# Kernel optimization log

Hardware: AMD Instinct MI355X
Metric: run time of the kernel (lower is better)

The kernel has to match this reference:

```python
import jax, jax.numpy as jnp
import numpy as np

N_NODES = 40000
N_EDGES = 640000
HIDDEN = 128
N_LAYERS = 4
N_CLASSES = 40
SCALING = HIDDEN ** -0.5  # num_heads = 1 -> head_dim = HIDDEN


def setup_inputs() -> dict:
    key = jax.random.key(0)
    ks = jax.random.split(key, 8)
    w_scale = HIDDEN ** -0.5
    h = jax.random.normal(ks[0], (N_NODES, HIDDEN), dtype=jnp.float32)
    src = jax.random.randint(ks[1], (N_EDGES,), 0, N_NODES, dtype=jnp.int32)
    dst = jnp.sort(jax.random.randint(ks[2], (N_EDGES,), 0, N_NODES, dtype=jnp.int32))
    Wq = jax.random.normal(ks[3], (N_LAYERS, HIDDEN, HIDDEN), dtype=jnp.float32) * w_scale
    Wk = jax.random.normal(ks[4], (N_LAYERS, HIDDEN, HIDDEN), dtype=jnp.float32) * w_scale
    Wv = jax.random.normal(ks[5], (N_LAYERS, HIDDEN, HIDDEN), dtype=jnp.float32) * w_scale
    bq = jnp.zeros((N_LAYERS, HIDDEN), dtype=jnp.float32)
    bk = jnp.zeros((N_LAYERS, HIDDEN), dtype=jnp.float32)
    bv = jnp.zeros((N_LAYERS, HIDDEN), dtype=jnp.float32)
    Wout = jax.random.normal(ks[6], (HIDDEN, N_CLASSES), dtype=jnp.float32) * w_scale
    bout = jnp.zeros((N_CLASSES,), dtype=jnp.float32)
    return {"h": h, "src": src, "dst": dst, "Wq": Wq, "bq": bq, "Wk": Wk,
            "bk": bk, "Wv": Wv, "bv": bv, "Wout": Wout, "bout": bout}


def _edge_softmax_spmm(q, k, v, src, dst):
    """Sparse MHA over graph edges (num_heads=1).
    score_e = <q[dst_e], k[src_e]>, softmax over incoming edges per dst,
    out[i] = sum_{e: dst_e = i} attn_e * v[src_e].
    """
    # SDDMM: [E]
    score = jnp.einsum('ed,ed->e', q[dst], k[src])
    # edge softmax over destination segments (stable)
    m = jax.ops.segment_max(score, dst, num_segments=N_NODES)  # [N]
    e = jnp.exp(score - m[dst])                                # [E]
    s = jax.ops.segment_sum(e, dst, num_segments=N_NODES)      # [N]
    attn = e / jnp.maximum(s[dst], 1e-20)                      # [E]
    # SpMM: [N, d]
    return jax.ops.segment_sum(attn[:, None] * v[src], dst, num_segments=N_NODES)


def reference(h, src, dst, Wq, bq, Wk, bk, Wv, bv, Wout, bout):
    for l in range(N_LAYERS):
        q = (h @ Wq[l] + bq[l]) * SCALING
        k = h @ Wk[l] + bk[l]
        v = h @ Wv[l] + bv[l]
        h = _edge_softmax_spmm(q, k, v, src, dst)
    logits = h @ Wout + bout
    return jax.nn.log_softmax(logits, axis=-1)
```

## Files before the change

kernel.cpp:

```cpp
#include <hip/hip_runtime.h>
#include <math.h>

#define N_NODES 40000
#define N_EDGES 640000
#define HIDDEN 128
#define N_LAYERS 4
#define N_CLASSES 40
#define SCALING 0.08838834764831845f

typedef __attribute__((ext_vector_type(8))) short short8;
typedef __attribute__((ext_vector_type(4))) float floatx4;

static __device__ __forceinline__ float b2f(unsigned short u) {
  return __uint_as_float(((unsigned)u) << 16);
}
static __device__ __forceinline__ unsigned short f2b(float f) {
  unsigned u = __float_as_uint(f);
  u += 0x7fff + ((u >> 16) & 1);
  return (unsigned short)(u >> 16);
}

__global__ __launch_bounds__(256) void setup_all(
    const float* __restrict__ h_in, const int* __restrict__ dst,
    const float* __restrict__ Wq, const float* __restrict__ Wk,
    const float* __restrict__ Wv, const float* __restrict__ Wout,
    unsigned short* __restrict__ hb0, int* __restrict__ row_start,
    unsigned short* __restrict__ Wqb, unsigned short* __restrict__ Wkb,
    unsigned short* __restrict__ Wvb, unsigned short* __restrict__ W2buf,
    unsigned short* __restrict__ wout_t)
{
  int idx = blockIdx.x * 256 + threadIdx.x;
  if (idx < 640000) {
    const float4* p = (const float4*)h_in + (size_t)idx * 2;
    float4 a = p[0], b = p[1];
    union { unsigned short us[8]; uint4 v; } o;
    o.us[0] = f2b(a.x); o.us[1] = f2b(a.y); o.us[2] = f2b(a.z); o.us[3] = f2b(a.w);
    o.us[4] = f2b(b.x); o.us[5] = f2b(b.y); o.us[6] = f2b(b.z); o.us[7] = f2b(b.w);
    ((uint4*)hb0)[idx] = o.v;
    return;
  }
  int j = idx - 640000;
  if (j < 65536) { Wqb[j] = f2b(Wq[j]); return; }
  if (j < 131072) { int i = j - 65536; Wkb[i] = f2b(Wk[i]); return; }
  if (j < 196608) { int i = j - 131072; Wvb[i] = f2b(Wv[i]); return; }
  if (j < 245760) {
    int i = j - 196608;
    int l = i >> 14, rem = i & 16383;
    int d = rem >> 7, kk = rem & 127;
    W2buf[(size_t)l * 32768 + (size_t)d * 128 + kk] =
        f2b(Wv[(size_t)l * 16384 + (size_t)kk * 128 + d]);
    return;
  }
  if (j < 251904) {
    int i = j - 245760;
    int c = i >> 7, d = i & 127;
    wout_t[i] = (c < N_CLASSES) ? f2b(Wout[(size_t)d * N_CLASSES + c]) : 0;
    return;
  }
  int c = j - 251904;
  if (c <= N_NODES) {
    int lo = 0, hi = N_EDGES;
    while (lo < hi) {
      int mid = (lo + hi) >> 1;
      if (dst[mid] < c) lo = mid + 1; else hi = mid;
    }
    row_start[c] = lo;
  }
}

__device__ __forceinline__ void mm_body(
    const unsigned short* __restrict__ Aop, const unsigned short* __restrict__ Bop,
    unsigned short* __restrict__ outp, int n_b, float scale)
{
  const int wid = threadIdx.x >> 6, lane = threadIdx.x & 63;
  const int r = lane & 15, kg = lane >> 4;
  const int row_base = wid * 32;

  int br0 = row_base + r;      if (br0 > n_b - 1) br0 = n_b - 1;
  int br1 = row_base + 16 + r; if (br1 > n_b - 1) br1 = n_b - 1;

  short8 bf_[2][4];
  #pragma unroll
  for (int kc = 0; kc < 4; ++kc) {
    bf_[0][kc] = *(const short8*)(Bop + (size_t)br0 * 128 + kc * 32 + kg * 8);
    bf_[1][kc] = *(const short8*)(Bop + (size_t)br1 * 128 + kc * 32 + kg * 8);
  }

  floatx4 acc[8][2];
  #pragma unroll
  for (int df = 0; df < 8; ++df) {
    acc[df][0] = (floatx4){0.f, 0.f, 0.f, 0.f};
    acc[df][1] = (floatx4){0.f, 0.f, 0.f, 0.f};
  }

  const unsigned short* ap = Aop + (size_t)r * 128 + kg * 8;
  #pragma unroll
  for (int df = 0; df < 8; ++df) {
    #pragma unroll
    for (int kc = 0; kc < 4; ++kc) {
      short8 af = *(const short8*)(ap + df * 2048 + kc * 32);
      acc[df][0] = __builtin_amdgcn_mfma_f32_16x16x32_bf16(af, bf_[0][kc], acc[df][0], 0, 0, 0);
      acc[df][1] = __builtin_amdgcn_mfma_f32_16x16x32_bf16(af, bf_[1][kc], acc[df][1], 0, 0, 0);
    }
  }

  #pragma unroll
  for (int df = 0; df < 8; ++df) {
    #pragma unroll
    for (int f = 0; f < 2; ++f) {
      int b = row_base + f * 16 + r;
      if (b < n_b) {
        union { unsigned short us[4]; uint2 u2; } o;
        o.us[0] = f2b(acc[df][f][0] * scale);
        o.us[1] = f2b(acc[df][f][1] * scale);
        o.us[2] = f2b(acc[df][f][2] * scale);
        o.us[3] = f2b(acc[df][f][3] * scale);
        *(uint2*)(outp + (size_t)b * 128 + df * 16 + kg * 4) = o.u2;
      }
    }
  }
}

__global__ __launch_bounds__(256) void mm_stage1(
    const unsigned short* __restrict__ Wqb, const unsigned short* __restrict__ Wkb,
    unsigned short* __restrict__ mts)
{
  int l = blockIdx.x;
  mm_body(Wqb + (size_t)l * 16384, Wkb + (size_t)l * 16384,
          mts + (size_t)l * 16384, 128, SCALING);
}

__global__ __launch_bounds__(256) void stage2_bias(
    const unsigned short* __restrict__ mts, const unsigned short* __restrict__ Wvb,
    const unsigned short* __restrict__ wout_t,
    unsigned short* __restrict__ W2buf, unsigned short* __restrict__ wout2,
    const float* __restrict__ bq, const float* __restrict__ Wk,
    const float* __restrict__ bv, const float* __restrict__ Wout,
    const float* __restrict__ bout,
    float* __restrict__ bqk0, float* __restrict__ bias2, float* __restrict__ bout2)
{
  int job = blockIdx.x;
  if (job < 3) {
    int l = job + 1;
    mm_body(Wvb + (size_t)(l - 1) * 16384, mts + (size_t)l * 16384,
            W2buf + (size_t)(l - 1) * 32768 + 16384, 128, 1.0f);
    return;
  }
  if (job == 3) {
    mm_body(Wvb + (size_t)3 * 16384, wout_t, wout2, 48, 1.0f);
    return;
  }
  int idx = (job - 4) * 256 + threadIdx.x;
  if (idx < 128) {
    int tp = idx;
    const float* wkrow = Wk + (size_t)tp * 128;
    float s = 0.f;
    #pragma unroll 4
    for (int j = 0; j < 128; ++j) s += bq[j] * wkrow[j];
    bqk0[tp] = s * SCALING;
  } else if (idx < 512) {
    int i = idx - 128;
    int l = (i >> 7) + 1, tp = i & 127;
    const unsigned short* mrow = mts + (size_t)l * 16384 + (size_t)tp * 128;
    const float* bvp = bv + (size_t)(l - 1) * 128;
    float s = 0.f;
    #pragma unroll 4
    for (int t = 0; t < 128; ++t) s += bvp[t] * b2f(mrow[t]);
    const float* bqp = bq + (size_t)l * 128;
    const float* wkrow = Wk + (size_t)l * 16384 + (size_t)tp * 128;
    float s2 = 0.f;
    #pragma unroll 4
    for (int j = 0; j < 128; ++j) s2 += bqp[j] * wkrow[j];
    bias2[(size_t)(l - 1) * 256 + 128 + tp] = s + s2 * SCALING;
  } else if (idx < 896) {
    int i = idx - 512;
    int l = (i >> 7) + 1, d = i & 127;
    bias2[(size_t)(l - 1) * 256 + d] = bv[(size_t)(l - 1) * 128 + d];
  } else if (idx < 944) {
    int c = idx - 896;
    float s = 0.f;
    #pragma unroll 4
    for (int d = 0; d < 128; ++d) s += bv[3 * 128 + d] * Wout[(size_t)d * N_CLASSES + c];
    bout2[c] = s + bout[c];
  }
}

template<int NCOLS>
__global__ __launch_bounds__(256) void gemm_qn(
    const unsigned short* __restrict__ A,
    const unsigned short* __restrict__ Wt,
    const float* __restrict__ bias,
    unsigned short* __restrict__ C)
{
  constexpr int HALF = NCOLS / 2;
  constexpr int NDF = HALF / 16;
  constexpr int ROWB = NCOLS * 2;
  __shared__ __align__(16) unsigned char cs[32 * ROWB];

  const int tid = threadIdx.x;
  const int wid = tid >> 6, lane = tid & 63;
  const int r = lane & 15, kg = lane >> 4;
  const int colhalf = wid & 1, rowsub = wid >> 1;
  const int colbase = colhalf * HALF;
  const int ro = rowsub * 16 + r;
  const int row = blockIdx.x * 32 + ro;

  short8 hf[4];
  #pragma unroll
  for (int kc = 0; kc < 4; ++kc)
    hf[kc] = *(const short8*)(A + (size_t)row * 128 + kc * 32 + kg * 8);

  floatx4 acc[NDF];
  #pragma unroll
  for (int df = 0; df < NDF; ++df) acc[df] = (floatx4){0.f, 0.f, 0.f, 0.f};

  const unsigned short* wp = Wt + (size_t)(colbase + r) * 128 + kg * 8;
  #pragma unroll
  for (int df = 0; df < NDF; ++df) {
    #pragma unroll
    for (int kc = 0; kc < 4; ++kc) {
      short8 wf = *(const short8*)(wp + df * 2048 + kc * 32);
      acc[df] = __builtin_amdgcn_mfma_f32_16x16x32_bf16(wf, hf[kc], acc[df], 0, 0, 0);
    }
  }

  #pragma unroll
  for (int df = 0; df < NDF; ++df) {
    float4 b4 = *(const float4*)&bias[colbase + df * 16 + kg * 4];
    union { unsigned short us[4]; uint2 u2; } o;
    o.us[0] = f2b(acc[df][0] + b4.x);
    o.us[1] = f2b(acc[df][1] + b4.y);
    o.us[2] = f2b(acc[df][2] + b4.z);
    o.us[3] = f2b(acc[df][3] + b4.w);
    int colb = (colbase + df * 16 + kg * 4) * 2;
    *(uint2*)(cs + ro * ROWB + (colb ^ ((ro & 7) << 4))) = o.u2;
  }
  __syncthreads();

  unsigned char* dstb = (unsigned char*)(C + (size_t)blockIdx.x * 32 * NCOLS);
  constexpr int NV = 32 * ROWB / 16;
  #pragma unroll
  for (int i = 0; i < NV / 256; ++i) {
    int byte = (i * 256 + tid) * 16;
    int ro2 = byte / ROWB;
    int colb2 = byte & (ROWB - 1);
    *(uint4*)(dstb + byte) =
        *(const uint4*)(cs + ro2 * ROWB + (colb2 ^ ((ro2 & 7) << 4)));
  }
}

template<int QSH, int HSH>
__global__ __launch_bounds__(128) void edge_fused(
    const unsigned short* __restrict__ qm, const unsigned short* __restrict__ h,
    const int* __restrict__ src, const int* __restrict__ row_start,
    unsigned short* __restrict__ g)
{
  const int lane = threadIdx.x & 63;
  const int node = blockIdx.x * 2 + (threadIdx.x >> 6);
  const int sg = lane >> 4, sl = lane & 15;

  short8 qf = *(const short8*)(qm + ((size_t)node << QSH) + sl * 8);
  float qd[8];
  #pragma unroll
  for (int j = 0; j < 8; ++j) qd[j] = b2f((unsigned short)qf[j]);

  const int r0 = row_start[node], r1 = row_start[node + 1];

  float acc[8] = {0.f, 0.f, 0.f, 0.f, 0.f, 0.f, 0.f, 0.f};
  float ws = 0.f;

#define LOADG(VLD, HF, C)                                               \
  {                                                                     \
    int e_ = (C) + sg;                                                  \
    VLD = e_ < r1;                                                      \
    int s_ = VLD ? src[e_] : 0;                                         \
    HF = *(const short8*)(h + ((size_t)s_ << HSH) + sl * 8);            \
  }

#define COMPG(VLD, HF)                                                  \
  {                                                                     \
    float hd_[8];                                                       \
    _Pragma("unroll")                                                   \
    for (int j = 0; j < 8; ++j) hd_[j] = b2f((unsigned short)HF[j]);    \
    float d0_ = 0.f, d1_ = 0.f;                                         \
    _Pragma("unroll")                                                   \
    for (int j = 0; j < 4; ++j) d0_ += qd[j] * hd_[j];                  \
    _Pragma("unroll")                                                   \
    for (int j = 4; j < 8; ++j) d1_ += qd[j] * hd_[j];                  \
    float d_ = d0_ + d1_;                                               \
    d_ += __shfl_xor(d_, 1, 64);                                        \
    d_ += __shfl_xor(d_, 2, 64);                                        \
    d_ += __shfl_xor(d_, 4, 64);                                        \
    d_ += __shfl_xor(d_, 8, 64);                                        \
    float w_ = VLD ? __expf(d_) : 0.f;                                  \
    ws += w_;                                                           \
    _Pragma("unroll")                                                   \
    for (int j = 0; j < 8; ++j) acc[j] += w_ * hd_[j];                  \
  }

  bool vA, vB;
  short8 hA, hB;
  LOADG(vA, hA, r0);
  LOADG(vB, hB, r0 + 4);

  for (int c = r0; c < r1; c += 8) {
    bool vC, vD;
    short8 hC, hD;
    LOADG(vC, hC, c + 8);
    LOADG(vD, hD, c + 12);
    COMPG(vA, hA);
    COMPG(vB, hB);
    vA = vC; hA = hC;
    vB = vD; hB = hD;
  }

#undef LOADG
#undef COMPG

  #pragma unroll
  for (int off = 16; off <= 32; off <<= 1) {
    ws += __shfl_xor(ws, off, 64);
    #pragma unroll
    for (int j = 0; j < 8; ++j) acc[j] += __shfl_xor(acc[j], off, 64);
  }

  if (sg == 0) {
    float inv = (ws > 1e-20f) ? 1.0f / ws : 0.0f;
    union { unsigned short us[8]; uint4 u4; } o;
    #pragma unroll
    for (int j = 0; j < 8; ++j) o.us[j] = f2b(acc[j] * inv);
    *(uint4*)(g + (size_t)node * 128 + sl * 8) = o.u4;
  }
}

__global__ __launch_bounds__(256) void out_head_mfma(
    const unsigned short* __restrict__ h, const unsigned short* __restrict__ wout_t,
    const float* __restrict__ bout, float* __restrict__ out)
{
  __shared__ __align__(16) float os[64 * N_CLASSES];

  const int wid = threadIdx.x >> 6, lane = threadIdx.x & 63;
  const int r = lane & 15, kg = lane >> 4;
  const int row_base = blockIdx.x * 64 + wid * 16;
  const int ar = row_base + r;

  floatx4 acc[3];
  #pragma unroll
  for (int n = 0; n < 3; ++n) acc[n] = (floatx4){0.f, 0.f, 0.f, 0.f};

  const unsigned short* ap = h + (size_t)ar * 128 + kg * 8;
  const unsigned short* bp = wout_t + (size_t)r * 128 + kg * 8;

  #pragma unroll
  for (int kc = 0; kc < 128; kc += 32) {
    short8 a0 = *(const short8*)(ap + kc);
    #pragma unroll
    for (int n = 0; n < 3; ++n) {
      short8 b = *(const short8*)(bp + n * 2048 + kc);
      acc[n] = __builtin_amdgcn_mfma_f32_16x16x32_bf16(a0, b, acc[n], 0, 0, 0);
    }
  }

  float bn0 = bout[r];
  float bn1 = bout[16 + r];
  float bn2 = (r < 8) ? bout[32 + r] : 0.f;

  #pragma unroll
  for (int g = 0; g < 4; ++g) {
    int rl = wid * 16 + kg * 4 + g;
    float l0 = acc[0][g] + bn0;
    float l1 = acc[1][g] + bn1;
    float l2 = acc[2][g] + bn2;
    float m = fmaxf(l0, l1);
    if (r < 8) m = fmaxf(m, l2);
    #pragma unroll
    for (int off = 8; off >= 1; off >>= 1) m = fmaxf(m, __shfl_xor(m, off, 64));
    float s = __expf(l0 - m) + __expf(l1 - m) + ((r < 8) ? __expf(l2 - m) : 0.f);
    #pragma unroll
    for (int off = 8; off >= 1; off >>= 1) s += __shfl_xor(s, off, 64);
    float lse = m + logf(s);
    os[rl * N_CLASSES + r]      = l0 - lse;
    os[rl * N_CLASSES + 16 + r] = l1 - lse;
    if (r < 8) os[rl * N_CLASSES + 32 + r] = l2 - lse;
  }
  __syncthreads();

  float* dstb = out + (size_t)blockIdx.x * 64 * N_CLASSES;
  #pragma unroll
  for (int i = 0; i < 3; ++i) {
    int idx = i * 256 + threadIdx.x;
    if (idx < 640)
      *(uint4*)(dstb + idx * 4) = *(const uint4*)(os + idx * 4);
  }
}

extern "C" void kernel_launch(void* const* d_in, const int* in_sizes, int n_in,
                              void* d_out, int out_size, void* d_ws, size_t ws_size,
                              hipStream_t stream) {
  const float* h_in = (const float*)d_in[0];
  const int*   src  = (const int*)d_in[1];
  const int*   dst  = (const int*)d_in[2];
  const float* Wq   = (const float*)d_in[3];
  const float* bq   = (const float*)d_in[4];
  const float* Wk   = (const float*)d_in[5];
  const float* bk   = (const float*)d_in[6];
  const float* Wv   = (const float*)d_in[7];
  const float* bv   = (const float*)d_in[8];
  const float* Wout = (const float*)d_in[9];
  const float* bout = (const float*)d_in[10];
  float* out = (float*)d_out;
  (void)bk;

  char* ws = (char*)d_ws;
  size_t off = 0;
  auto alloc = [&](size_t bytes) -> void* {
    void* p = ws + off;
    off += (bytes + 255) & ~(size_t)255;
    return p;
  };
  int*            row_start = (int*)           alloc((size_t)(N_NODES + 1) * sizeof(int));
  unsigned short* hb0       = (unsigned short*)alloc((size_t)N_NODES * 128 * 2);
  unsigned short* qm0       = (unsigned short*)alloc((size_t)N_NODES * 128 * 2);
  unsigned short* g0        = (unsigned short*)alloc((size_t)N_NODES * 128 * 2);
  unsigned short* g1        = (unsigned short*)alloc((size_t)N_NODES * 128 * 2);
  unsigned short* hq        = (unsigned short*)alloc((size_t)N_NODES * 256 * 2);
  unsigned short* mts       = (unsigned short*)alloc((size_t)4 * 16384 * 2);
  unsigned short* W2buf     = (unsigned short*)alloc((size_t)3 * 32768 * 2);
  unsigned short* wout2     = (unsigned short*)alloc((size_t)48 * 128 * 2);
  unsigned short* Wqb       = (unsigned short*)alloc((size_t)4 * 16384 * 2);
  unsigned short* Wkb       = (unsigned short*)alloc((size_t)4 * 16384 * 2);
  unsigned short* Wvb       = (unsigned short*)alloc((size_t)4 * 16384 * 2);
  unsigned short* wout_t    = (unsigned short*)alloc((size_t)48 * 128 * 2);
  float*          bqk0      = (float*)         alloc(128 * sizeof(float));
  float*          bias2     = (float*)         alloc(3 * 256 * sizeof(float));
  float*          bout2     = (float*)         alloc(48 * sizeof(float));

  setup_all<<<3641, 256, 0, stream>>>(h_in, dst, Wq, Wk, Wv, Wout,
                                      hb0, row_start, Wqb, Wkb, Wvb, W2buf, wout_t);
  mm_stage1<<<4, 256, 0, stream>>>(Wqb, Wkb, mts);
  stage2_bias<<<8, 256, 0, stream>>>(mts, Wvb, wout_t, W2buf, wout2,
                                     bq, Wk, bv, Wout, bout, bqk0, bias2, bout2);

  gemm_qn<128><<<1250, 256, 0, stream>>>(hb0, mts, bqk0, qm0);
  edge_fused<7, 7><<<N_NODES / 2, 128, 0, stream>>>(qm0, hb0, src, row_start, g0);
  unsigned short* gprev = g0;
  unsigned short* gnext = g1;
  for (int l = 1; l < N_LAYERS; ++l) {
    gemm_qn<256><<<1250, 256, 0, stream>>>(
        gprev, W2buf + (size_t)(l - 1) * 32768, bias2 + (size_t)(l - 1) * 256, hq);
    edge_fused<8, 8><<<N_NODES / 2, 128, 0, stream>>>(hq + 128, hq, src, row_start, gnext);
    unsigned short* tmp = gprev; gprev = gnext; gnext = tmp;
  }
  out_head_mfma<<<625, 256, 0, stream>>>(gprev, wout2, bout2, out);
}
```

Baseline: 251.0 us.

## Fold value projections into cumulative weight chain, gather raw features per layer

```diff
diff --git a/kernel.cpp b/kernel.cpp
--- a/kernel.cpp
+++ b/kernel.cpp
@@ -22,12 +22,7 @@
 
 __global__ __launch_bounds__(256) void setup_all(
     const float* __restrict__ h_in, const int* __restrict__ dst,
-    const float* __restrict__ Wq, const float* __restrict__ Wk,
-    const float* __restrict__ Wv, const float* __restrict__ Wout,
-    unsigned short* __restrict__ hb0, int* __restrict__ row_start,
-    unsigned short* __restrict__ Wqb, unsigned short* __restrict__ Wkb,
-    unsigned short* __restrict__ Wvb, unsigned short* __restrict__ W2buf,
-    unsigned short* __restrict__ wout_t)
+    unsigned short* __restrict__ g0, int* __restrict__ row_start)
 {
   int idx = blockIdx.x * 256 + threadIdx.x;
   if (idx < 640000) {
@@ -36,28 +31,10 @@
     union { unsigned short us[8]; uint4 v; } o;
     o.us[0] = f2b(a.x); o.us[1] = f2b(a.y); o.us[2] = f2b(a.z); o.us[3] = f2b(a.w);
     o.us[4] = f2b(b.x); o.us[5] = f2b(b.y); o.us[6] = f2b(b.z); o.us[7] = f2b(b.w);
-    ((uint4*)hb0)[idx] = o.v;
+    ((uint4*)g0)[idx] = o.v;
     return;
   }
-  int j = idx - 640000;
-  if (j < 65536) { Wqb[j] = f2b(Wq[j]); return; }
-  if (j < 131072) { int i = j - 65536; Wkb[i] = f2b(Wk[i]); return; }
-  if (j < 196608) { int i = j - 131072; Wvb[i] = f2b(Wv[i]); return; }
-  if (j < 245760) {
-    int i = j - 196608;
-    int l = i >> 14, rem = i & 16383;
-    int d = rem >> 7, kk = rem & 127;
-    W2buf[(size_t)l * 32768 + (size_t)d * 128 + kk] =
-        f2b(Wv[(size_t)l * 16384 + (size_t)kk * 128 + d]);
-    return;
-  }
-  if (j < 251904) {
-    int i = j - 245760;
-    int c = i >> 7, d = i & 127;
-    wout_t[i] = (c < N_CLASSES) ? f2b(Wout[(size_t)d * N_CLASSES + c]) : 0;
-    return;
-  }
-  int c = j - 251904;
+  int c = idx - 640000;
   if (c <= N_NODES) {
     int lo = 0, hi = N_EDGES;
     while (lo < hi) {
@@ -68,140 +45,116 @@
   }
 }
 
-__device__ __forceinline__ void mm_body(
-    const unsigned short* __restrict__ Aop, const unsigned short* __restrict__ Bop,
-    unsigned short* __restrict__ outp, int n_b, float scale)
+struct MMJob {
+  const float* A; const float* B;
+  float* Cf; unsigned short* Cb;
+  float scale;
+  int abt; int ncolsB; int storeT; int padrows;
+};
+struct MMStage { MMJob jobs[4]; int njobs; int bias; };
+
+__global__ __launch_bounds__(256) void mm_stage(
+    MMStage st,
+    const float* __restrict__ Wq, const float* __restrict__ Wk,
+    const float* __restrict__ Wv, const float* __restrict__ Wout,
+    const float* __restrict__ bq, const float* __restrict__ bv,
+    const float* __restrict__ bout,
+    const float* __restrict__ C2, const float* __restrict__ C3,
+    float* __restrict__ zb, float* __restrict__ bout2)
 {
-  const int wid = threadIdx.x >> 6, lane = threadIdx.x & 63;
-  const int r = lane & 15, kg = lane >> 4;
-  const int row_base = wid * 32;
-
-  int br0 = row_base + r;      if (br0 > n_b - 1) br0 = n_b - 1;
-  int br1 = row_base + 16 + r; if (br1 > n_b - 1) br1 = n_b - 1;
-
-  short8 bf_[2][4];
-  #pragma unroll
-  for (int kc = 0; kc < 4; ++kc) {
-    bf_[0][kc] = *(const short8*)(Bop + (size_t)br0 * 128 + kc * 32 + kg * 8);
-    bf_[1][kc] = *(const short8*)(Bop + (size_t)br1 * 128 + kc * 32 + kg * 8);
-  }
-
-  floatx4 acc[8][2];
-  #pragma unroll
-  for (int df = 0; df < 8; ++df) {
-    acc[df][0] = (floatx4){0.f, 0.f, 0.f, 0.f};
-    acc[df][1] = (floatx4){0.f, 0.f, 0.f, 0.f};
-  }
-
-  const unsigned short* ap = Aop + (size_t)r * 128 + kg * 8;
-  #pragma unroll
-  for (int df = 0; df < 8; ++df) {
-    #pragma unroll
-    for (int kc = 0; kc < 4; ++kc) {
-      short8 af = *(const short8*)(ap + df * 2048 + kc * 32);
-      acc[df][0] = __builtin_amdgcn_mfma_f32_16x16x32_bf16(af, bf_[0][kc], acc[df][0], 0, 0, 0);
-      acc[df][1] = __builtin_amdgcn_mfma_f32_16x16x32_bf16(af, bf_[1][kc], acc[df][1], 0, 0, 0);
-    }
-  }
-
-  #pragma unroll
-  for (int df = 0; df < 8; ++df) {
-    #pragma unroll
-    for (int f = 0; f < 2; ++f) {
-      int b = row_base + f * 16 + r;
-      if (b < n_b) {
-        union { unsigned short us[4]; uint2 u2; } o;
-        o.us[0] = f2b(acc[df][f][0] * scale);
-        o.us[1] = f2b(acc[df][f][1] * scale);
-        o.us[2] = f2b(acc[df][f][2] * scale);
-        o.us[3] = f2b(acc[df][f][3] * scale);
-        *(uint2*)(outp + (size_t)b * 128 + df * 16 + kg * 4) = o.u2;
+  int blk = blockIdx.x;
+  if (blk < st.njobs * 64) {
+    MMJob J = st.jobs[blk >> 6];
+    int bi = blk & 63;
+    int ty = threadIdx.x >> 7;
+    int c  = threadIdx.x & 127;
+    int r  = bi * 2 + ty;
+    float acc = 0.f;
+    if (J.abt) {
+      const float* ar = J.A + (size_t)r * 128;
+      const float* br = J.B + (size_t)c * 128;
+      #pragma unroll 4
+      for (int j = 0; j < 128; ++j) acc += ar[j] * br[j];
+    } else if (c < J.ncolsB) {
+      const float* ar = J.A + (size_t)r * 128;
+      #pragma unroll 4
+      for (int j = 0; j < 128; ++j) acc += ar[j] * J.B[(size_t)j * J.ncolsB + c];
+    }
+    acc *= J.scale;
+    if (J.storeT) {
+      if (c < J.ncolsB) {
+        if (J.Cb) J.Cb[(size_t)c * 128 + r] = f2b(acc);
+        else      J.Cf[(size_t)c * 128 + r] = acc;
+      } else if (c < J.padrows && J.Cb) {
+        J.Cb[(size_t)c * 128 + r] = 0;
       }
-    }
-  }
-}
-
-__global__ __launch_bounds__(256) void mm_stage1(
-    const unsigned short* __restrict__ Wqb, const unsigned short* __restrict__ Wkb,
-    unsigned short* __restrict__ mts)
-{
-  int l = blockIdx.x;
-  mm_body(Wqb + (size_t)l * 16384, Wkb + (size_t)l * 16384,
-          mts + (size_t)l * 16384, 128, SCALING);
-}
-
-__global__ __launch_bounds__(256) void stage2_bias(
-    const unsigned short* __restrict__ mts, const unsigned short* __restrict__ Wvb,
-    const unsigned short* __restrict__ wout_t,
-    unsigned short* __restrict__ W2buf, unsigned short* __restrict__ wout2,
-    const float* __restrict__ bq, const float* __restrict__ Wk,
-    const float* __restrict__ bv, const float* __restrict__ Wout,
-    const float* __restrict__ bout,
-    float* __restrict__ bqk0, float* __restrict__ bias2, float* __restrict__ bout2)
-{
-  int job = blockIdx.x;
-  if (job < 3) {
-    int l = job + 1;
-    mm_body(Wvb + (size_t)(l - 1) * 16384, mts + (size_t)l * 16384,
-            W2buf + (size_t)(l - 1) * 32768 + 16384, 128, 1.0f);
+    } else if (c < J.ncolsB) {
+      if (J.Cb) J.Cb[(size_t)r * J.ncolsB + c] = f2b(acc);
+      else      J.Cf[(size_t)r * J.ncolsB + c] = acc;
+    }
     return;
   }
-  if (job == 3) {
-    mm_body(Wvb + (size_t)3 * 16384, wout_t, wout2, 48, 1.0f);
-    return;
-  }
-  int idx = (job - 4) * 256 + threadIdx.x;
-  if (idx < 128) {
-    int tp = idx;
-    const float* wkrow = Wk + (size_t)tp * 128;
+  if (!st.bias) return;
+
+  int t = threadIdx.x;
+  __shared__ float cb[128], v1[128], v2[128], cbn[128];
+  if (t < 128) {
+    const float* wk0 = Wk + (size_t)t * 128;
     float s = 0.f;
-    #pragma unroll 4
-    for (int j = 0; j < 128; ++j) s += bq[j] * wkrow[j];
-    bqk0[tp] = s * SCALING;
-  } else if (idx < 512) {
-    int i = idx - 128;
-    int l = (i >> 7) + 1, tp = i & 127;
-    const unsigned short* mrow = mts + (size_t)l * 16384 + (size_t)tp * 128;
-    const float* bvp = bv + (size_t)(l - 1) * 128;
-    float s = 0.f;
-    #pragma unroll 4
-    for (int t = 0; t < 128; ++t) s += bvp[t] * b2f(mrow[t]);
-    const float* bqp = bq + (size_t)l * 128;
-    const float* wkrow = Wk + (size_t)l * 16384 + (size_t)tp * 128;
-    float s2 = 0.f;
-    #pragma unroll 4
-    for (int j = 0; j < 128; ++j) s2 += bqp[j] * wkrow[j];
-    bias2[(size_t)(l - 1) * 256 + 128 + tp] = s + s2 * SCALING;
-  } else if (idx < 896) {
-    int i = idx - 512;
-    int l = (i >> 7) + 1, d = i & 127;
-    bias2[(size_t)(l - 1) * 256 + d] = bv[(size_t)(l - 1) * 128 + d];
-  } else if (idx < 944) {
-    int c = idx - 896;
-    float s = 0.f;
-    #pragma unroll 4
-    for (int d = 0; d < 128; ++d) s += bv[3 * 128 + d] * Wout[(size_t)d * N_CLASSES + c];
-    bout2[c] = s + bout[c];
-  }
-}
-
-template<int NCOLS>
-__global__ __launch_bounds__(256) void gemm_qn(
+    for (int o = 0; o < 128; ++o) s += bq[o] * wk0[o];
+    zb[t] = s * SCALING;
+    cb[t] = bv[t];
+  }
+  __syncthreads();
+  for (int l = 1; l < 4; ++l) {
+    const float* Cvl = (l == 1) ? Wv : (l == 2 ? C2 : C3);
+    if (t < 128) {
+      float s = bq[(size_t)l * 128 + t];
+      for (int o = 0; o < 128; ++o) s += cb[o] * Wq[(size_t)l * 16384 + (size_t)o * 128 + t];
+      v1[t] = s;
+    }
+    __syncthreads();
+    if (t < 128) {
+      float s = 0.f;
+      const float* wkr = Wk + (size_t)l * 16384 + (size_t)t * 128;
+      for (int o = 0; o < 128; ++o) s += v1[o] * wkr[o];
+      v2[t] = s;
+    }
+    __syncthreads();
+    if (t < 128) {
+      float s = 0.f;
+      const float* cvr = Cvl + (size_t)t * 128;
+      for (int d = 0; d < 128; ++d) s += v2[d] * cvr[d];
+      zb[(size_t)l * 128 + t] = s * SCALING;
+      float s2 = bv[(size_t)l * 128 + t];
+      for (int d = 0; d < 128; ++d) s2 += cb[d] * Wv[(size_t)l * 16384 + (size_t)d * 128 + t];
+      cbn[t] = s2;
+    }
+    __syncthreads();
+    if (t < 128) cb[t] = cbn[t];
+    __syncthreads();
+  }
+  if (t < N_CLASSES) {
+    float s = bout[t];
+    for (int d = 0; d < 128; ++d) s += cb[d] * Wout[(size_t)d * N_CLASSES + t];
+    bout2[t] = s;
+  }
+}
+
+__global__ __launch_bounds__(256) void gemm_z(
     const unsigned short* __restrict__ A,
     const unsigned short* __restrict__ Wt,
     const float* __restrict__ bias,
     unsigned short* __restrict__ C)
 {
-  constexpr int HALF = NCOLS / 2;
-  constexpr int NDF = HALF / 16;
-  constexpr int ROWB = NCOLS * 2;
+  constexpr int ROWB = 256;
   __shared__ __align__(16) unsigned char cs[32 * ROWB];
 
   const int tid = threadIdx.x;
   const int wid = tid >> 6, lane = tid & 63;
   const int r = lane & 15, kg = lane >> 4;
   const int colhalf = wid & 1, rowsub = wid >> 1;
-  const int colbase = colhalf * HALF;
+  const int colbase = colhalf * 64;
   const int ro = rowsub * 16 + r;
   const int row = blockIdx.x * 32 + ro;
 
@@ -210,13 +163,13 @@
   for (int kc = 0; kc < 4; ++kc)
     hf[kc] = *(const short8*)(A + (size_t)row * 128 + kc * 32 + kg * 8);
 
-  floatx4 acc[NDF];
-  #pragma unroll
-  for (int df = 0; df < NDF; ++df) acc[df] = (floatx4){0.f, 0.f, 0.f, 0.f};
+  floatx4 acc[4];
+  #pragma unroll
+  for (int df = 0; df < 4; ++df) acc[df] = (floatx4){0.f, 0.f, 0.f, 0.f};
 
   const unsigned short* wp = Wt + (size_t)(colbase + r) * 128 + kg * 8;
   #pragma unroll
-  for (int df = 0; df < NDF; ++df) {
+  for (int df = 0; df < 4; ++df) {
     #pragma unroll
     for (int kc = 0; kc < 4; ++kc) {
       short8 wf = *(const short8*)(wp + df * 2048 + kc * 32);
@@ -225,7 +178,7 @@
   }
 
   #pragma unroll
-  for (int df = 0; df < NDF; ++df) {
+  for (int df = 0; df < 4; ++df) {
     float4 b4 = *(const float4*)&bias[colbase + df * 16 + kg * 4];
     union { unsigned short us[4]; uint2 u2; } o;
     o.us[0] = f2b(acc[df][0] + b4.x);
@@ -237,10 +190,9 @@
   }
   __syncthreads();
 
-  unsigned char* dstb = (unsigned char*)(C + (size_t)blockIdx.x * 32 * NCOLS);
-  constexpr int NV = 32 * ROWB / 16;
-  #pragma unroll
-  for (int i = 0; i < NV / 256; ++i) {
+  unsigned char* dstb = (unsigned char*)(C + (size_t)blockIdx.x * 32 * 128);
+  #pragma unroll
+  for (int i = 0; i < 2; ++i) {
     int byte = (i * 256 + tid) * 16;
     int ro2 = byte / ROWB;
     int colb2 = byte & (ROWB - 1);
@@ -249,17 +201,16 @@
   }
 }
 
-template<int QSH, int HSH>
 __global__ __launch_bounds__(128) void edge_fused(
-    const unsigned short* __restrict__ qm, const unsigned short* __restrict__ h,
+    const unsigned short* __restrict__ z, const unsigned short* __restrict__ g,
     const int* __restrict__ src, const int* __restrict__ row_start,
-    unsigned short* __restrict__ g)
+    unsigned short* __restrict__ gout)
 {
   const int lane = threadIdx.x & 63;
   const int node = blockIdx.x * 2 + (threadIdx.x >> 6);
   const int sg = lane >> 4, sl = lane & 15;
 
-  short8 qf = *(const short8*)(qm + ((size_t)node << QSH) + sl * 8);
+  short8 qf = *(const short8*)(z + ((size_t)node << 7) + sl * 8);
   float qd[8];
   #pragma unroll
   for (int j = 0; j < 8; ++j) qd[j] = b2f((unsigned short)qf[j]);
@@ -274,7 +225,7 @@
     int e_ = (C) + sg;                                                  \
     VLD = e_ < r1;                                                      \
     int s_ = VLD ? src[e_] : 0;                                         \
-    HF = *(const short8*)(h + ((size_t)s_ << HSH) + sl * 8);            \
+    HF = *(const short8*)(g + ((size_t)s_ << 7) + sl * 8);              \
   }
 
 #define COMPG(VLD, HF)                                                  \
@@ -329,7 +280,7 @@
     union { unsigned short us[8]; uint4 u4; } o;
     #pragma unroll
     for (int j = 0; j < 8; ++j) o.us[j] = f2b(acc[j] * inv);
-    *(uint4*)(g + (size_t)node * 128 + sl * 8) = o.u4;
+    *(uint4*)(gout + (size_t)node * 128 + sl * 8) = o.u4;
   }
 }
 
@@ -419,37 +370,68 @@
     return p;
   };
   int*            row_start = (int*)           alloc((size_t)(N_NODES + 1) * sizeof(int));
-  unsigned short* hb0       = (unsigned short*)alloc((size_t)N_NODES * 128 * 2);
-  unsigned short* qm0       = (unsigned short*)alloc((size_t)N_NODES * 128 * 2);
   unsigned short* g0        = (unsigned short*)alloc((size_t)N_NODES * 128 * 2);
   unsigned short* g1        = (unsigned short*)alloc((size_t)N_NODES * 128 * 2);
-  unsigned short* hq        = (unsigned short*)alloc((size_t)N_NODES * 256 * 2);
-  unsigned short* mts       = (unsigned short*)alloc((size_t)4 * 16384 * 2);
-  unsigned short* W2buf     = (unsigned short*)alloc((size_t)3 * 32768 * 2);
-  unsigned short* wout2     = (unsigned short*)alloc((size_t)48 * 128 * 2);
-  unsigned short* Wqb       = (unsigned short*)alloc((size_t)4 * 16384 * 2);
-  unsigned short* Wkb       = (unsigned short*)alloc((size_t)4 * 16384 * 2);
-  unsigned short* Wvb       = (unsigned short*)alloc((size_t)4 * 16384 * 2);
-  unsigned short* wout_t    = (unsigned short*)alloc((size_t)48 * 128 * 2);
-  float*          bqk0      = (float*)         alloc(128 * sizeof(float));
-  float*          bias2     = (float*)         alloc(3 * 256 * sizeof(float));
-  float*          bout2     = (float*)         alloc(48 * sizeof(float));
-
-  setup_all<<<3641, 256, 0, stream>>>(h_in, dst, Wq, Wk, Wv, Wout,
-                                      hb0, row_start, Wqb, Wkb, Wvb, W2buf, wout_t);
-  mm_stage1<<<4, 256, 0, stream>>>(Wqb, Wkb, mts);
-  stage2_bias<<<8, 256, 0, stream>>>(mts, Wvb, wout_t, W2buf, wout2,
-                                     bq, Wk, bv, Wout, bout, bqk0, bias2, bout2);
-
-  gemm_qn<128><<<1250, 256, 0, stream>>>(hb0, mts, bqk0, qm0);
-  edge_fused<7, 7><<<N_NODES / 2, 128, 0, stream>>>(qm0, hb0, src, row_start, g0);
-  unsigned short* gprev = g0;
+  unsigned short* zbuf      = (unsigned short*)alloc((size_t)N_NODES * 128 * 2);
+  unsigned short* WZ        = (unsigned short*)alloc((size_t)4 * 16384 * 2);
+  unsigned short* WOt       = (unsigned short*)alloc((size_t)48 * 128 * 2);
+  float*          C2        = (float*)alloc(16384 * sizeof(float));
+  float*          C3        = (float*)alloc(16384 * sizeof(float));
+  float*          C4        = (float*)alloc(16384 * sizeof(float));
+  float*          Abuf      = (float*)alloc(3 * 16384 * sizeof(float));
+  float*          Bbuf      = (float*)alloc(3 * 16384 * sizeof(float));
+  float*          zb        = (float*)alloc(4 * 128 * sizeof(float));
+  float*          bout2     = (float*)alloc(64 * sizeof(float));
+
+  setup_all<<<(680001 + 255) / 256, 256, 0, stream>>>(h_in, dst, g0, row_start);
+
+  auto J = [](const float* A, const float* B, float* Cf, unsigned short* Cb,
+              float scale, int abt, int ncolsB, int storeT, int padrows) {
+    MMJob j; j.A = A; j.B = B; j.Cf = Cf; j.Cb = Cb; j.scale = scale;
+    j.abt = abt; j.ncolsB = ncolsB; j.storeT = storeT; j.padrows = padrows;
+    return j;
+  };
+  const float* Wq_l[4] = {Wq, Wq + 16384, Wq + 32768, Wq + 49152};
+  const float* Wk_l[4] = {Wk, Wk + 16384, Wk + 32768, Wk + 49152};
+  const float* Wv_l[4] = {Wv, Wv + 16384, Wv + 32768, Wv + 49152};
+
+  MMStage s0 = {};
+  s0.jobs[0] = J(Wk_l[0], Wq_l[0], nullptr, WZ, SCALING, 1, 128, 0, 0);
+  s0.jobs[1] = J(Wv_l[0], Wv_l[1], C2, nullptr, 1.f, 0, 128, 0, 0);
+  s0.jobs[2] = J(Wv_l[0], Wk_l[1], Abuf, nullptr, 1.f, 0, 128, 0, 0);
+  s0.jobs[3] = J(Wv_l[0], Wq_l[1], Bbuf, nullptr, 1.f, 0, 128, 0, 0);
+  s0.njobs = 4; s0.bias = 0;
+
+  MMStage s1 = {};
+  s1.jobs[0] = J(Abuf, Bbuf, nullptr, WZ + 16384, SCALING, 1, 128, 0, 0);
+  s1.jobs[1] = J(C2, Wv_l[2], C3, nullptr, 1.f, 0, 128, 0, 0);
+  s1.jobs[2] = J(C2, Wk_l[2], Abuf + 16384, nullptr, 1.f, 0, 128, 0, 0);
+  s1.jobs[3] = J(C2, Wq_l[2], Bbuf + 16384, nullptr, 1.f, 0, 128, 0, 0);
+  s1.njobs = 4; s1.bias = 0;
+
+  MMStage s2 = {};
+  s2.jobs[0] = J(Abuf + 16384, Bbuf + 16384, nullptr, WZ + 32768, SCALING, 1, 128, 0, 0);
+  s2.jobs[1] = J(C3, Wv_l[3], C4, nullptr, 1.f, 0, 128, 0, 0);
+  s2.jobs[2] = J(C3, Wk_l[3], Abuf + 32768, nullptr, 1.f, 0, 128, 0, 0);
+  s2.jobs[3] = J(C3, Wq_l[3], Bbuf + 32768, nullptr, 1.f, 0, 128, 0, 0);
+  s2.njobs = 4; s2.bias = 0;
+
+  MMStage s3 = {};
+  s3.jobs[0] = J(Abuf + 32768, Bbuf + 32768, nullptr, WZ + 49152, SCALING, 1, 128, 0, 0);
+  s3.jobs[1] = J(C4, Wout, nullptr, WOt, 1.f, 0, N_CLASSES, 1, 48);
+  s3.njobs = 2; s3.bias = 1;
+
+  mm_stage<<<4 * 64, 256, 0, stream>>>(s0, Wq, Wk, Wv, Wout, bq, bv, bout, C2, C3, zb, bout2);
+  mm_stage<<<4 * 64, 256, 0, stream>>>(s1, Wq, Wk, Wv, Wout, bq, bv, bout, C2, C3, zb, bout2);
+  mm_stage<<<4 * 64, 256, 0, stream>>>(s2, Wq, Wk, Wv, Wout, bq, bv, bout, C2, C3, zb, bout2);
+  mm_stage<<<2 * 64 + 1, 256, 0, stream>>>(s3, Wq, Wk, Wv, Wout, bq, bv, bout, C2, C3, zb, bout2);
+
+  unsigned short* gcur = g0;
   unsigned short* gnext = g1;
-  for (int l = 1; l < N_LAYERS; ++l) {
-    gemm_qn<256><<<1250, 256, 0, stream>>>(
-        gprev, W2buf + (size_t)(l - 1) * 32768, bias2 + (size_t)(l - 1) * 256, hq);
-    edge_fused<8, 8><<<N_NODES / 2, 128, 0, stream>>>(hq + 128, hq, src, row_start, gnext);
-    unsigned short* tmp = gprev; gprev = gnext; gnext = tmp;
-  }
-  out_head_mfma<<<625, 256, 0, stream>>>(gprev, wout2, bout2, out);
-}
+  for (int l = 0; l < N_LAYERS; ++l) {
+    gemm_z<<<1250, 256, 0, stream>>>(gcur, WZ + (size_t)l * 16384, zb + (size_t)l * 128, zbuf);
+    edge_fused<<<N_NODES / 2, 128, 0, stream>>>(zbuf, gcur, src, row_start, gnext);
+    unsigned short* tmp = gcur; gcur = gnext; gnext = tmp;
+  }
+  out_head_mfma<<<625, 256, 0, stream>>>(gcur, WOt, bout2, out);
+}
```

Result: no change. 251.5 us (+0.2%).
